# Kernel tuning notes

Measured on AMD Instinct MI355X. Metric: run time of the kernel, lower is better.

## Reference

```python
import jax, jax.numpy as jnp
import numpy as np

HIDDEN = 512


def setup_inputs() -> dict:
    key = jax.random.key(0)
    ks = jax.random.split(key, 5)
    S, B, I, H = 256, 128, 1024, HIDDEN
    scale_ih = 1.0 / np.sqrt(H)
    return {
        "x": jax.random.normal(ks[0], (S, B, I), dtype=jnp.float32),
        "w_ih": jax.random.normal(ks[1], (4 * H, I), dtype=jnp.float32) * scale_ih,
        "w_hh": jax.random.normal(ks[2], (4 * H, H), dtype=jnp.float32) * scale_ih,
        "b_ih": jax.random.normal(ks[3], (4 * H,), dtype=jnp.float32) * scale_ih,
        "b_hh": jax.random.normal(ks[4], (4 * H,), dtype=jnp.float32) * scale_ih,
    }


def reference(x, w_ih, w_hh, b_ih, b_hh):
    # x: [S, B, I]. LSTMCell with PyTorch gate order (i, f, g, o).
    S, B, _ = x.shape
    H = HIDDEN
    bias = b_ih + b_hh  # fuse both biases

    def step(carry, xt):
        h, c = carry
        gates = xt @ w_ih.T + h @ w_hh.T + bias  # [B, 4H]
        i, f, g, o = jnp.split(gates, 4, axis=-1)
        i = jax.nn.sigmoid(i)
        f = jax.nn.sigmoid(f)
        g = jnp.tanh(g)
        o = jax.nn.sigmoid(o)
        c = f * c + i * g
        h = o * jnp.tanh(c)
        # original code's h[arange(B)] / c[arange(B)] is an identity gather: no-op
        return (h, c), None

    h0 = jnp.zeros((B, H), dtype=x.dtype)
    c0 = jnp.zeros((B, H), dtype=x.dtype)
    (h, c), _ = jax.lax.scan(step, (h0, c0), x)
    return h.sum()
```

## Files before the change

### kernel.cpp

```cpp
#include <hip/hip_runtime.h>

typedef __attribute__((ext_vector_type(8))) short short8;
typedef __attribute__((ext_vector_type(4))) float f32x4;

#define S_LEN 256
#define BATCH 128
#define IN_DIM 1024
#define HID 512
#define G4 2048

#define SENT 0xFFFFFFFFu

__device__ __forceinline__ unsigned short f32_bf16(float f) {
  unsigned int u = __float_as_uint(f);
  u = (u + 0x7FFFu + ((u >> 16) & 1u)) >> 16;
  return (unsigned short)u;
}
__device__ __forceinline__ float bf16_f32(unsigned short h) {
  return __uint_as_float(((unsigned int)h) << 16);
}
__device__ __forceinline__ float sigm(float x) { return 1.0f / (1.0f + __expf(-x)); }
__device__ __forceinline__ float tanh_fast(float x) {
  return 1.0f - 2.0f / (__expf(2.0f * x) + 1.0f);
}

__global__ void cvt_bf16(const float* __restrict__ src, unsigned short* __restrict__ dst, int n) {
  int i = (blockIdx.x * blockDim.x + threadIdx.x) * 4;
  if (i >= n) return;
  float4 v = *(const float4*)(src + i);
  ushort4 o;
  o.x = f32_bf16(v.x); o.y = f32_bf16(v.y); o.z = f32_bf16(v.z); o.w = f32_bf16(v.w);
  *(ushort4*)(dst + i) = o;
}

__global__ void init_all(const float* __restrict__ b_ih, const float* __restrict__ b_hh,
                         float* __restrict__ bias, uint4* __restrict__ hring4) {
  int i = blockIdx.x * blockDim.x + threadIdx.x;
  if (i < G4) bias[i] = b_ih[i] + b_hh[i];
  const int SLOT4 = BATCH * HID / 8;
  const int TOT4 = 257 * SLOT4;
  const uint4 z = make_uint4(0u, 0u, 0u, 0u);
  const uint4 sN = make_uint4(SENT, SENT, SENT, SENT);
  for (int k = i; k < TOT4; k += gridDim.x * blockDim.x)
    hring4[k] = (k < SLOT4) ? z : sN;
}

__device__ __forceinline__ void gl_lds16(const void* g, void* l) {
  __builtin_amdgcn_global_load_lds(
      (const __attribute__((address_space(1))) unsigned int*)g,
      (__attribute__((address_space(3))) unsigned int*)l, 16, 0, 0);
}

template <int C_F32>
__global__ __launch_bounds__(256) void gemm_bias(
    const unsigned short* __restrict__ A,
    const unsigned short* __restrict__ Bw,
    const float* __restrict__ bias,
    void* __restrict__ Cout) {
  __shared__ __align__(16) unsigned short As[128 * 32];
  __shared__ __align__(16) unsigned short Bs[128 * 32];
  const int tid = threadIdx.x;
  const int w = tid >> 6, l = tid & 63;
  const int wm = w & 1, wn = w >> 1;
  const int nt = blockIdx.x & 15, mt = blockIdx.x >> 4;

  f32x4 acc[4][4];
#pragma unroll
  for (int i = 0; i < 4; i++)
#pragma unroll
    for (int j = 0; j < 4; j++) acc[i][j] = f32x4{0.f, 0.f, 0.f, 0.f};

  for (int k0 = 0; k0 < 1024; k0 += 32) {
    __syncthreads();
#pragma unroll
    for (int jj = 0; jj < 2; jj++) {
      int cid = (w * 2 + jj) * 64 + l;
      int row = cid >> 2, kc = cid & 3;
      const unsigned short* ga = A + (size_t)(mt * 128 + row) * 1024 + k0 + kc * 8;
      gl_lds16(ga, As + (w * 2 + jj) * 512);
      const unsigned short* gb = Bw + (size_t)(nt * 128 + row) * 1024 + k0 + kc * 8;
      gl_lds16(gb, Bs + (w * 2 + jj) * 512);
    }
    __syncthreads();
    short8 a[4], b[4];
#pragma unroll
    for (int i = 0; i < 4; i++)
      a[i] = *(const short8*)&As[(wm * 64 + i * 16 + (l & 15)) * 32 + (l >> 4) * 8];
#pragma unroll
    for (int j = 0; j < 4; j++)
      b[j] = *(const short8*)&Bs[(wn * 64 + j * 16 + (l & 15)) * 32 + (l >> 4) * 8];
#pragma unroll
    for (int i = 0; i < 4; i++)
#pragma unroll
      for (int j = 0; j < 4; j++)
        acc[i][j] = __builtin_amdgcn_mfma_f32_16x16x32_bf16(a[i], b[j], acc[i][j], 0, 0, 0);
  }
#pragma unroll
  for (int j = 0; j < 4; j++) {
    int cg = nt * 128 + wn * 64 + j * 16 + (l & 15);
    float bv = bias[cg];
#pragma unroll
    for (int i = 0; i < 4; i++) {
      int rbase = mt * 128 + wm * 64 + i * 16 + (l >> 4) * 4;
#pragma unroll
      for (int r = 0; r < 4; r++) {
        float v = acc[i][j][r] + bv;
        if (C_F32)
          ((float*)Cout)[(size_t)(rbase + r) * 2048 + cg] = v;
        else
          ((unsigned short*)Cout)[(size_t)(rbase + r) * 2048 + cg] = f32_bf16(v);
      }
    }
  }
}

__global__ __launch_bounds__(256, 1) void lstm_rec(
    const unsigned short* __restrict__ whh,
    const void* __restrict__ gx,
    int gx_f32,
    unsigned* __restrict__ hring) {
  __shared__ __align__(16) unsigned short Hs[2][16][520];
  __shared__ __align__(16) float Gt[16][132];

  const int tid = threadIdx.x;
  const int w = tid >> 6, l = tid & 63;
  const int m = blockIdx.x & 7;
  const int s = blockIdx.x >> 3;

  short8 bw[16][2];
#pragma unroll
  for (int u = 0; u < 2; u++) {
    int n = (2 * w + u) * 16 + (l & 15);
    int jn = n >> 2, g = n & 3;
    int R = g * 512 + s * 32 + jn;
    const unsigned short* base = whh + (size_t)R * 512 + ((l >> 4) * 8);
#pragma unroll
    for (int kk = 0; kk < 16; kk++) bw[kk][u] = *(const short8*)(base + kk * 32);
  }

  const int b = l & 15;
  const int p = 4 * w + (l >> 4);
  const int gb = m * 16 + b;
  const int colg = s * 32 + 2 * p;
  float c0 = 0.f, c1 = 0.f;

  const float* gxf = (const float*)gx;
  const unsigned short* gxb = (const unsigned short*)gx;
  const int SLOTW = BATCH * HID / 2;
  const unsigned long long* hull = (const unsigned long long*)hring;
  const int SLOTQ = BATCH * HID / 4;

  const int skc = tid & 127;
  const int srow = tid >> 7;
  const bool selfst = (((tid >> 3) & 15) == s);

  unsigned long long v[8];
#pragma unroll
  for (int it = 0; it < 8; it++)
    v[it] = __hip_atomic_load(&hull[(size_t)(m * 16 + it * 2 + srow) * 128 + skc],
                              __ATOMIC_RELAXED, __HIP_MEMORY_SCOPE_AGENT);
  float2 pg[4];
  {
    size_t base0 = (size_t)gb * G4 + colg;
    if (gx_f32) {
#pragma unroll
      for (int g = 0; g < 4; g++) pg[g] = *(const float2*)(gxf + base0 + (size_t)g * 512);
    } else {
#pragma unroll
      for (int g = 0; g < 4; g++) {
        unsigned u = *(const unsigned*)(gxb + base0 + (size_t)g * 512);
        pg[g].x = bf16_f32((unsigned short)(u & 0xFFFFu));
        pg[g].y = bf16_f32((unsigned short)(u >> 16));
      }
    }
  }

  for (int t = 0; t < S_LEN; t++) {
    const int buf = t & 1;
    const unsigned long long* src = hull + (size_t)t * SLOTQ;

    if (!(selfst && t > 0)) {
      for (;;) {
        int bad = 0;
#pragma unroll
        for (int it = 0; it < 8; it++)
          bad |= (((unsigned)v[it] == SENT) | ((unsigned)(v[it] >> 32) == SENT)) << it;
        if (!bad) break;
#pragma unroll
        for (int it = 0; it < 8; it++)
          if ((bad >> it) & 1)
            v[it] = __hip_atomic_load(&src[(size_t)(m * 16 + it * 2 + srow) * 128 + skc],
                                      __ATOMIC_RELAXED, __HIP_MEMORY_SCOPE_AGENT);
      }
#pragma unroll
      for (int it = 0; it < 8; it++)
        *(unsigned long long*)&Hs[buf][it * 2 + srow][skc * 4] = v[it];
    }
    __syncthreads();

    unsigned long long vn[8];
    float2 pgn[4];
    if (t + 1 < S_LEN) {
      if (!selfst) {
        const unsigned long long* srcn = hull + (size_t)(t + 1) * SLOTQ;
#pragma unroll
        for (int it = 0; it < 8; it++)
          vn[it] = __hip_atomic_load(&srcn[(size_t)(m * 16 + it * 2 + srow) * 128 + skc],
                                     __ATOMIC_RELAXED, __HIP_MEMORY_SCOPE_AGENT);
      }
      size_t basen = (size_t)((t + 1) * BATCH + gb) * G4 + colg;
      if (gx_f32) {
#pragma unroll
        for (int g = 0; g < 4; g++) pgn[g] = *(const float2*)(gxf + basen + (size_t)g * 512);
      } else {
#pragma unroll
        for (int g = 0; g < 4; g++) {
          unsigned u = *(const unsigned*)(gxb + basen + (size_t)g * 512);
          pgn[g].x = bf16_f32((unsigned short)(u & 0xFFFFu));
          pgn[g].y = bf16_f32((unsigned short)(u >> 16));
        }
      }
    }

    f32x4 acc0 = f32x4{0.f, 0.f, 0.f, 0.f};
    f32x4 acc1 = f32x4{0.f, 0.f, 0.f, 0.f};
#pragma unroll
    for (int kk = 0; kk < 16; kk++) {
      short8 a = *(const short8*)&Hs[buf][l & 15][kk * 32 + (l >> 4) * 8];
      acc0 = __builtin_amdgcn_mfma_f32_16x16x32_bf16(a, bw[kk][0], acc0, 0, 0, 0);
      acc1 = __builtin_amdgcn_mfma_f32_16x16x32_bf16(a, bw[kk][1], acc1, 0, 0, 0);
    }

#pragma unroll
    for (int r = 0; r < 4; r++) {
      Gt[(l >> 4) * 4 + r][(2 * w + 0) * 16 + (l & 15)] = acc0[r];
      Gt[(l >> 4) * 4 + r][(2 * w + 1) * 16 + (l & 15)] = acc1[r];
    }

    float4 g0 = *(const float4*)&Gt[b][8 * p];
    float4 g1 = *(const float4*)&Gt[b][8 * p + 4];
    float i0 = sigm(g0.x + pg[0].x), f0 = sigm(g0.y + pg[1].x);
    float gg0 = tanh_fast(g0.z + pg[2].x), o0 = sigm(g0.w + pg[3].x);
    c0 = f0 * c0 + i0 * gg0;
    float h0 = o0 * tanh_fast(c0);
    float i1 = sigm(g1.x + pg[0].y), f1 = sigm(g1.y + pg[1].y);
    float gg1 = tanh_fast(g1.z + pg[2].y), o1 = sigm(g1.w + pg[3].y);
    c1 = f1 * c1 + i1 * gg1;
    float h1 = o1 * tanh_fast(c1);
    unsigned hp = (unsigned)f32_bf16(h0) | ((unsigned)f32_bf16(h1) << 16);

    __hip_atomic_store(&hring[(size_t)(t + 1) * SLOTW + gb * 256 + s * 16 + p], hp,
                       __ATOMIC_RELAXED, __HIP_MEMORY_SCOPE_AGENT);
    *(unsigned*)&Hs[buf ^ 1][b][colg] = hp;

#pragma unroll
    for (int it = 0; it < 8; it++) v[it] = vn[it];
#pragma unroll
    for (int g = 0; g < 4; g++) pg[g] = pgn[g];
  }
}

__global__ void reduce_sum(const unsigned short* __restrict__ h, float* __restrict__ out) {
  __shared__ float red[256];
  int tid = threadIdx.x;
  float s = 0.f;
  for (int i = tid * 8; i < BATCH * HID; i += 256 * 8) {
    uint4 v = *(const uint4*)(h + i);
    unsigned int q[4] = {v.x, v.y, v.z, v.w};
#pragma unroll
    for (int k = 0; k < 4; k++) {
      s += bf16_f32((unsigned short)(q[k] & 0xFFFFu));
      s += bf16_f32((unsigned short)(q[k] >> 16));
    }
  }
  red[tid] = s;
  __syncthreads();
  for (int off = 128; off > 0; off >>= 1) {
    if (tid < off) red[tid] += red[tid + off];
    __syncthreads();
  }
  if (tid == 0) out[0] = red[0];
}

extern "C" void kernel_launch(void* const* d_in, const int* in_sizes, int n_in,
                              void* d_out, int out_size, void* d_ws, size_t ws_size,
                              hipStream_t stream) {
  const float* x = (const float*)d_in[0];
  const float* w_ih = (const float*)d_in[1];
  const float* w_hh = (const float*)d_in[2];
  const float* b_ih = (const float*)d_in[3];
  const float* b_hh = (const float*)d_in[4];

  char* ws = (char*)d_ws;
  unsigned short* x_bf = (unsigned short*)(ws);
  unsigned short* wih_bf = (unsigned short*)(ws + 67108864);
  unsigned short* whh_bf = (unsigned short*)(ws + 71303168);
  float* bias = (float*)(ws + 73400320);
  unsigned* hring = (unsigned*)(ws + 73408512);
  void* gx = (void*)(ws + 107094016);

  const size_t need_f32 = 107094016ull + (size_t)S_LEN * BATCH * G4 * 4;
  int gx_f32 = (ws_size >= need_f32) ? 1 : 0;

  cvt_bf16<<<(33554432 / 4 + 255) / 256, 256, 0, stream>>>(x, x_bf, 33554432);
  cvt_bf16<<<(2097152 / 4 + 255) / 256, 256, 0, stream>>>(w_ih, wih_bf, 2097152);
  cvt_bf16<<<(1048576 / 4 + 255) / 256, 256, 0, stream>>>(w_hh, whh_bf, 1048576);
  init_all<<<256, 256, 0, stream>>>(b_ih, b_hh, bias, (uint4*)hring);

  if (gx_f32)
    gemm_bias<1><<<4096, 256, 0, stream>>>(x_bf, wih_bf, bias, gx);
  else
    gemm_bias<0><<<4096, 256, 0, stream>>>(x_bf, wih_bf, bias, gx);

  void* args[] = {(void*)&whh_bf, (void*)&gx, (void*)&gx_f32, (void*)&hring};
  hipLaunchCooperativeKernel((const void*)lstm_rec, dim3(128), dim3(256), args, 0, stream);

  reduce_sum<<<1, 256, 0, stream>>>((const unsigned short*)(hring + 256 * (BATCH * HID / 2)),
                                    (float*)d_out);
}
```

Baseline: 1.201 ms.

## Fuse input-projection GEMM into recurrent kernel with per-timestep readiness counters

Merges the separate input-projection GEMM and the cooperative recurrence into one persistent kernel. 128 worker blocks compute the x·W_ih tiles timestep by timestep and bump a per-timestep counter, while the 128 recurrence blocks spin on that counter before reading the projected gates. The GEMM now uses 128x256 tiles with double-buffered LDS staging. The projected gates are always stored in bf16 instead of fp32 when workspace allowed, so the overlap comes with some precision risk and extra polling and synchronization overhead on the latency-critical recurrence path.

```diff
diff --git a/kernel.cpp b/kernel.cpp
--- a/kernel.cpp
+++ b/kernel.cpp
@@ -11,6 +11,14 @@
 
 #define SENT 0xFFFFFFFFu
 
+#define LSTM_BLOCKS 128
+#define GEMM_WORKERS 128
+#define TOT_BLOCKS (LSTM_BLOCKS + GEMM_WORKERS)
+#define NT_PER_ROW 8
+#define N_TILES (256 * NT_PER_ROW)
+
+__device__ unsigned g_cnt[S_LEN];
+
 __device__ __forceinline__ unsigned short f32_bf16(float f) {
   unsigned int u = __float_as_uint(f);
   u = (u + 0x7FFFu + ((u >> 16) & 1u)) >> 16;
@@ -22,6 +30,12 @@
 __device__ __forceinline__ float sigm(float x) { return 1.0f / (1.0f + __expf(-x)); }
 __device__ __forceinline__ float tanh_fast(float x) {
   return 1.0f - 2.0f / (__expf(2.0f * x) + 1.0f);
+}
+__device__ __forceinline__ unsigned ld_cnt(const unsigned* p) {
+  return __hip_atomic_load(p, __ATOMIC_RELAXED, __HIP_MEMORY_SCOPE_AGENT);
+}
+__device__ __forceinline__ unsigned ld_u32_agent(const void* p) {
+  return __hip_atomic_load((const unsigned*)p, __ATOMIC_RELAXED, __HIP_MEMORY_SCOPE_AGENT);
 }
 
 __global__ void cvt_bf16(const float* __restrict__ src, unsigned short* __restrict__ dst, int n) {
@@ -37,6 +51,7 @@
                          float* __restrict__ bias, uint4* __restrict__ hring4) {
   int i = blockIdx.x * blockDim.x + threadIdx.x;
   if (i < G4) bias[i] = b_ih[i] + b_hh[i];
+  if (i < S_LEN) g_cnt[i] = 0u;
   const int SLOT4 = BATCH * HID / 8;
   const int TOT4 = 257 * SLOT4;
   const uint4 z = make_uint4(0u, 0u, 0u, 0u);
@@ -51,79 +66,100 @@
       (__attribute__((address_space(3))) unsigned int*)l, 16, 0, 0);
 }
 
-template <int C_F32>
-__global__ __launch_bounds__(256) void gemm_bias(
-    const unsigned short* __restrict__ A,
-    const unsigned short* __restrict__ Bw,
+__global__ __launch_bounds__(512, 1) void fused_lstm(
+    const unsigned short* __restrict__ whh,
+    const unsigned short* __restrict__ xbf,
+    const unsigned short* __restrict__ wih,
     const float* __restrict__ bias,
-    void* __restrict__ Cout) {
-  __shared__ __align__(16) unsigned short As[128 * 32];
-  __shared__ __align__(16) unsigned short Bs[128 * 32];
+    unsigned short* __restrict__ gx,
+    unsigned* __restrict__ hring) {
+  __shared__ __align__(16) union {
+    struct { unsigned short Hs[2][16][520]; float Gt[16][132]; } L;
+    struct { unsigned short As[2 * 4096]; unsigned short Bs[2 * 8192]; } G;
+  } sm;
+
   const int tid = threadIdx.x;
   const int w = tid >> 6, l = tid & 63;
-  const int wm = w & 1, wn = w >> 1;
-  const int nt = blockIdx.x & 15, mt = blockIdx.x >> 4;
-
-  f32x4 acc[4][4];
-#pragma unroll
-  for (int i = 0; i < 4; i++)
-#pragma unroll
-    for (int j = 0; j < 4; j++) acc[i][j] = f32x4{0.f, 0.f, 0.f, 0.f};
-
-  for (int k0 = 0; k0 < 1024; k0 += 32) {
-    __syncthreads();
-#pragma unroll
-    for (int jj = 0; jj < 2; jj++) {
-      int cid = (w * 2 + jj) * 64 + l;
-      int row = cid >> 2, kc = cid & 3;
-      const unsigned short* ga = A + (size_t)(mt * 128 + row) * 1024 + k0 + kc * 8;
-      gl_lds16(ga, As + (w * 2 + jj) * 512);
-      const unsigned short* gb = Bw + (size_t)(nt * 128 + row) * 1024 + k0 + kc * 8;
-      gl_lds16(gb, Bs + (w * 2 + jj) * 512);
-    }
-    __syncthreads();
-    short8 a[4], b[4];
-#pragma unroll
-    for (int i = 0; i < 4; i++)
-      a[i] = *(const short8*)&As[(wm * 64 + i * 16 + (l & 15)) * 32 + (l >> 4) * 8];
-#pragma unroll
-    for (int j = 0; j < 4; j++)
-      b[j] = *(const short8*)&Bs[(wn * 64 + j * 16 + (l & 15)) * 32 + (l >> 4) * 8];
-#pragma unroll
-    for (int i = 0; i < 4; i++)
-#pragma unroll
-      for (int j = 0; j < 4; j++)
-        acc[i][j] = __builtin_amdgcn_mfma_f32_16x16x32_bf16(a[i], b[j], acc[i][j], 0, 0, 0);
-  }
-#pragma unroll
-  for (int j = 0; j < 4; j++) {
-    int cg = nt * 128 + wn * 64 + j * 16 + (l & 15);
-    float bv = bias[cg];
-#pragma unroll
-    for (int i = 0; i < 4; i++) {
-      int rbase = mt * 128 + wm * 64 + i * 16 + (l >> 4) * 4;
-#pragma unroll
-      for (int r = 0; r < 4; r++) {
-        float v = acc[i][j][r] + bv;
-        if (C_F32)
-          ((float*)Cout)[(size_t)(rbase + r) * 2048 + cg] = v;
-        else
-          ((unsigned short*)Cout)[(size_t)(rbase + r) * 2048 + cg] = f32_bf16(v);
-      }
-    }
-  }
-}
-
-__global__ __launch_bounds__(256, 1) void lstm_rec(
-    const unsigned short* __restrict__ whh,
-    const void* __restrict__ gx,
-    int gx_f32,
-    unsigned* __restrict__ hring) {
-  __shared__ __align__(16) unsigned short Hs[2][16][520];
-  __shared__ __align__(16) float Gt[16][132];
-
-  const int tid = threadIdx.x;
-  const int w = tid >> 6, l = tid & 63;
+
+  if (blockIdx.x >= LSTM_BLOCKS) {
+    const int wm = w & 1, wn = w >> 1;
+    for (int tile = (int)blockIdx.x - LSTM_BLOCKS; tile < N_TILES; tile += GEMM_WORKERS) {
+      const int nt = tile & (NT_PER_ROW - 1), mt = tile >> 3;
+      f32x4 acc[4][4];
+#pragma unroll
+      for (int i = 0; i < 4; i++)
+#pragma unroll
+        for (int j = 0; j < 4; j++) acc[i][j] = f32x4{0.f, 0.f, 0.f, 0.f};
+
+      auto stage = [&](int cur, int k0) {
+        {
+          int row = tid >> 2, kc = tid & 3;
+          gl_lds16(xbf + (size_t)(mt * 128 + row) * 1024 + k0 + kc * 8,
+                   sm.G.As + cur * 4096 + w * 512);
+        }
+#pragma unroll
+        for (int jj = 0; jj < 2; ++jj) {
+          int cid = jj * 512 + tid;
+          int row = cid >> 2, kc = cid & 3;
+          gl_lds16(wih + (size_t)(nt * 256 + row) * 1024 + k0 + kc * 8,
+                   sm.G.Bs + cur * 8192 + jj * 4096 + w * 512);
+        }
+      };
+
+      stage(0, 0);
+      asm volatile("s_waitcnt vmcnt(0)" ::: "memory");
+      __builtin_amdgcn_s_barrier();
+
+      for (int ks = 0; ks < 32; ++ks) {
+        const int cur = ks & 1;
+        if (ks + 1 < 32) stage(cur ^ 1, (ks + 1) * 32);
+        short8 a[4], b[4];
+#pragma unroll
+        for (int i = 0; i < 4; i++)
+          a[i] = *(const short8*)&sm.G.As[cur * 4096 +
+                                          (wm * 64 + i * 16 + (l & 15)) * 32 + (l >> 4) * 8];
+#pragma unroll
+        for (int j = 0; j < 4; j++)
+          b[j] = *(const short8*)&sm.G.Bs[cur * 8192 +
+                                          (wn * 64 + j * 16 + (l & 15)) * 32 + (l >> 4) * 8];
+#pragma unroll
+        for (int i = 0; i < 4; i++)
+#pragma unroll
+          for (int j = 0; j < 4; j++)
+            acc[i][j] = __builtin_amdgcn_mfma_f32_16x16x32_bf16(a[i], b[j], acc[i][j], 0, 0, 0);
+        __builtin_amdgcn_sched_barrier(0);
+        asm volatile("s_waitcnt vmcnt(0)" ::: "memory");
+        __builtin_amdgcn_s_barrier();
+      }
+
+#pragma unroll
+      for (int j = 0; j < 4; j++) {
+        int cg = nt * 256 + wn * 64 + j * 16 + (l & 15);
+        float bv = bias[cg];
+#pragma unroll
+        for (int i = 0; i < 4; i++) {
+          int rbase = mt * 128 + wm * 64 + i * 16 + (l >> 4) * 4;
+#pragma unroll
+          for (int r = 0; r < 4; r++) {
+            unsigned short hv = f32_bf16(acc[i][j][r] + bv);
+            __hip_atomic_store(gx + (size_t)(rbase + r) * G4 + cg, hv,
+                               __ATOMIC_RELAXED, __HIP_MEMORY_SCOPE_AGENT);
+          }
+        }
+      }
+      asm volatile("s_waitcnt vmcnt(0)" ::: "memory");
+      __syncthreads();
+      if (tid == 0)
+        __hip_atomic_fetch_add(&g_cnt[mt], 1u, __ATOMIC_RELAXED, __HIP_MEMORY_SCOPE_AGENT);
+    }
+    return;
+  }
+
+  __builtin_amdgcn_s_setprio(1);
+  if (tid >= 256) {
+    for (int t = 0; t < S_LEN; t++) __syncthreads();
+    return;
+  }
   const int m = blockIdx.x & 7;
   const int s = blockIdx.x >> 3;
 
@@ -144,8 +180,6 @@
   const int colg = s * 32 + 2 * p;
   float c0 = 0.f, c1 = 0.f;
 
-  const float* gxf = (const float*)gx;
-  const unsigned short* gxb = (const unsigned short*)gx;
   const int SLOTW = BATCH * HID / 2;
   const unsigned long long* hull = (const unsigned long long*)hring;
   const int SLOTQ = BATCH * HID / 4;
@@ -159,21 +193,18 @@
   for (int it = 0; it < 8; it++)
     v[it] = __hip_atomic_load(&hull[(size_t)(m * 16 + it * 2 + srow) * 128 + skc],
                               __ATOMIC_RELAXED, __HIP_MEMORY_SCOPE_AGENT);
+  while (ld_cnt(&g_cnt[0]) != (unsigned)NT_PER_ROW) __builtin_amdgcn_s_sleep(2);
   float2 pg[4];
   {
     size_t base0 = (size_t)gb * G4 + colg;
-    if (gx_f32) {
-#pragma unroll
-      for (int g = 0; g < 4; g++) pg[g] = *(const float2*)(gxf + base0 + (size_t)g * 512);
-    } else {
-#pragma unroll
-      for (int g = 0; g < 4; g++) {
-        unsigned u = *(const unsigned*)(gxb + base0 + (size_t)g * 512);
-        pg[g].x = bf16_f32((unsigned short)(u & 0xFFFFu));
-        pg[g].y = bf16_f32((unsigned short)(u >> 16));
-      }
-    }
-  }
+#pragma unroll
+    for (int g = 0; g < 4; g++) {
+      unsigned u = ld_u32_agent(gx + base0 + (size_t)g * 512);
+      pg[g].x = bf16_f32((unsigned short)(u & 0xFFFFu));
+      pg[g].y = bf16_f32((unsigned short)(u >> 16));
+    }
+  }
+  unsigned cn = ld_cnt(&g_cnt[1]);
 
   for (int t = 0; t < S_LEN; t++) {
     const int buf = t & 1;
@@ -194,7 +225,7 @@
       }
 #pragma unroll
       for (int it = 0; it < 8; it++)
-        *(unsigned long long*)&Hs[buf][it * 2 + srow][skc * 4] = v[it];
+        *(unsigned long long*)&sm.L.Hs[buf][it * 2 + srow][skc * 4] = v[it];
     }
     __syncthreads();
 
@@ -208,37 +239,39 @@
           vn[it] = __hip_atomic_load(&srcn[(size_t)(m * 16 + it * 2 + srow) * 128 + skc],
                                      __ATOMIC_RELAXED, __HIP_MEMORY_SCOPE_AGENT);
       }
+      if (cn != (unsigned)NT_PER_ROW) {
+        do {
+          __builtin_amdgcn_s_sleep(1);
+          cn = ld_cnt(&g_cnt[t + 1]);
+        } while (cn != (unsigned)NT_PER_ROW);
+      }
       size_t basen = (size_t)((t + 1) * BATCH + gb) * G4 + colg;
-      if (gx_f32) {
-#pragma unroll
-        for (int g = 0; g < 4; g++) pgn[g] = *(const float2*)(gxf + basen + (size_t)g * 512);
-      } else {
-#pragma unroll
-        for (int g = 0; g < 4; g++) {
-          unsigned u = *(const unsigned*)(gxb + basen + (size_t)g * 512);
-          pgn[g].x = bf16_f32((unsigned short)(u & 0xFFFFu));
-          pgn[g].y = bf16_f32((unsigned short)(u >> 16));
-        }
-      }
+#pragma unroll
+      for (int g = 0; g < 4; g++) {
+        unsigned u = ld_u32_agent(gx + basen + (size_t)g * 512);
+        pgn[g].x = bf16_f32((unsigned short)(u & 0xFFFFu));
+        pgn[g].y = bf16_f32((unsigned short)(u >> 16));
+      }
+      cn = (t + 2 < S_LEN) ? ld_cnt(&g_cnt[t + 2]) : (unsigned)NT_PER_ROW;
     }
 
     f32x4 acc0 = f32x4{0.f, 0.f, 0.f, 0.f};
     f32x4 acc1 = f32x4{0.f, 0.f, 0.f, 0.f};
 #pragma unroll
     for (int kk = 0; kk < 16; kk++) {
-      short8 a = *(const short8*)&Hs[buf][l & 15][kk * 32 + (l >> 4) * 8];
+      short8 a = *(const short8*)&sm.L.Hs[buf][l & 15][kk * 32 + (l >> 4) * 8];
       acc0 = __builtin_amdgcn_mfma_f32_16x16x32_bf16(a, bw[kk][0], acc0, 0, 0, 0);
       acc1 = __builtin_amdgcn_mfma_f32_16x16x32_bf16(a, bw[kk][1], acc1, 0, 0, 0);
     }
 
 #pragma unroll
     for (int r = 0; r < 4; r++) {
-      Gt[(l >> 4) * 4 + r][(2 * w + 0) * 16 + (l & 15)] = acc0[r];
-      Gt[(l >> 4) * 4 + r][(2 * w + 1) * 16 + (l & 15)] = acc1[r];
-    }
-
-    float4 g0 = *(const float4*)&Gt[b][8 * p];
-    float4 g1 = *(const float4*)&Gt[b][8 * p + 4];
+      sm.L.Gt[(l >> 4) * 4 + r][(2 * w + 0) * 16 + (l & 15)] = acc0[r];
+      sm.L.Gt[(l >> 4) * 4 + r][(2 * w + 1) * 16 + (l & 15)] = acc1[r];
+    }
+
+    float4 g0 = *(const float4*)&sm.L.Gt[b][8 * p];
+    float4 g1 = *(const float4*)&sm.L.Gt[b][8 * p + 4];
     float i0 = sigm(g0.x + pg[0].x), f0 = sigm(g0.y + pg[1].x);
     float gg0 = tanh_fast(g0.z + pg[2].x), o0 = sigm(g0.w + pg[3].x);
     c0 = f0 * c0 + i0 * gg0;
@@ -251,7 +284,7 @@
 
     __hip_atomic_store(&hring[(size_t)(t + 1) * SLOTW + gb * 256 + s * 16 + p], hp,
                        __ATOMIC_RELAXED, __HIP_MEMORY_SCOPE_AGENT);
-    *(unsigned*)&Hs[buf ^ 1][b][colg] = hp;
+    *(unsigned*)&sm.L.Hs[buf ^ 1][b][colg] = hp;
 
 #pragma unroll
     for (int it = 0; it < 8; it++) v[it] = vn[it];
@@ -297,23 +330,17 @@
   unsigned short* whh_bf = (unsigned short*)(ws + 71303168);
   float* bias = (float*)(ws + 73400320);
   unsigned* hring = (unsigned*)(ws + 73408512);
-  void* gx = (void*)(ws + 107094016);
-
-  const size_t need_f32 = 107094016ull + (size_t)S_LEN * BATCH * G4 * 4;
-  int gx_f32 = (ws_size >= need_f32) ? 1 : 0;
+  unsigned short* gx = (unsigned short*)(ws + 107094016);
 
   cvt_bf16<<<(33554432 / 4 + 255) / 256, 256, 0, stream>>>(x, x_bf, 33554432);
   cvt_bf16<<<(2097152 / 4 + 255) / 256, 256, 0, stream>>>(w_ih, wih_bf, 2097152);
   cvt_bf16<<<(1048576 / 4 + 255) / 256, 256, 0, stream>>>(w_hh, whh_bf, 1048576);
   init_all<<<256, 256, 0, stream>>>(b_ih, b_hh, bias, (uint4*)hring);
 
-  if (gx_f32)
-    gemm_bias<1><<<4096, 256, 0, stream>>>(x_bf, wih_bf, bias, gx);
-  else
-    gemm_bias<0><<<4096, 256, 0, stream>>>(x_bf, wih_bf, bias, gx);
-
-  void* args[] = {(void*)&whh_bf, (void*)&gx, (void*)&gx_f32, (void*)&hring};
-  hipLaunchCooperativeKernel((const void*)lstm_rec, dim3(128), dim3(256), args, 0, stream);
+  void* args[] = {(void*)&whh_bf, (void*)&x_bf, (void*)&wih_bf,
+                  (void*)&bias, (void*)&gx, (void*)&hring};
+  hipLaunchCooperativeKernel((const void*)fused_lstm, dim3(TOT_BLOCKS), dim3(512), args, 0,
+                             stream);
 
   reduce_sum<<<1, 256, 0, stream>>>((const unsigned short*)(hring + 256 * (BATCH * HID / 2)),
                                     (float*)d_out);
```

After: 1.119 ms. -6.8%, faster.
